# Kernel tuning notes

Measured on AMD Instinct MI355X. Metric: run time of the kernel, lower is better.

The kernel has to match this reference:

```python
import jax, jax.numpy as jnp
import numpy as np

B, C, T, L, H = 4, 512, 8, 512, 8


def _normalize(a, eps=1e-12):
    # F.normalize: x / max(||x||_2, eps) along last dim
    n = jnp.linalg.norm(a, axis=-1, keepdims=True)
    return a / jnp.maximum(n, eps)


def setup_inputs() -> dict:
    key = jax.random.key(0)
    ks = jax.random.split(key, 8)
    w = lambda k, shp: (jax.random.normal(k, shp, dtype=jnp.float32) * 0.02)
    return {
        "e": jax.random.normal(ks[0], (B, C, T, L), dtype=jnp.float32),
        "x": jax.random.normal(ks[1], (B, C, T, L), dtype=jnp.float32),
        "Wq": w(ks[2], (C, C)), "bq": jnp.zeros((C,), jnp.float32),
        "Wkv": w(ks[3], (2 * C, C)), "bkv": jnp.zeros((2 * C,), jnp.float32),
        "Wm": w(ks[4], (C, C)), "bm": jnp.zeros((C,), jnp.float32),
        "Wg1": w(ks[5], (C, C)), "bg1": jnp.zeros((C,), jnp.float32),
        "Wg2": w(ks[6], (H, C)), "bg2": jnp.zeros((H,), jnp.float32),
    }


def reference(e, x, Wq, bq, Wkv, bkv, Wm, bm, Wg1, bg1, Wg2, bg2):
    shortcut = x
    xp = jnp.transpose(x, (0, 2, 3, 1))  # (b,t,l,c)
    ep = jnp.transpose(e, (0, 2, 3, 1))  # (b,t,l,c)
    b, t, l, c = xp.shape
    hd = c // H

    # per-(b,t) head gating from pooled e (gate_weights1 == gate_weights in source)
    pooled = ep.mean(axis=2)  # (b,t,c)
    glog = jnp.tanh(pooled @ Wg1.T + bg1) @ Wg2.T + bg2  # (b,t,H)
    gw = jax.nn.softmax(glog, axis=-1)[..., None, None]  # (b,t,H,1,1)

    q = (ep @ Wq.T + bq).reshape(b, t, l, H, hd).transpose(0, 1, 3, 2, 4)  # (b,t,H,l,hd)
    q = _normalize(q)
    kv = (xp @ Wkv.T + bkv).reshape(b, t, l, 2 * H, hd).transpose(0, 1, 3, 2, 4)
    k, v = kv[:, :, :H], kv[:, :, H:]
    k = _normalize(k)
    v = _normalize(v) * gw  # pre-softmax value gating

    scale = jnp.float32(1.0 / np.sqrt(hd))
    att = jax.nn.softmax(jnp.einsum('bthid,bthjd->bthij', q, k) * scale, axis=-1)
    o = jnp.einsum('bthij,bthjd->bthid', att, v) * gw  # post-attention gating

    o = o.transpose(0, 1, 3, 2, 4).reshape(b, t, l, c)
    o = o @ Wm.T + bm
    return jnp.transpose(o, (0, 3, 1, 2)) + shortcut
```

## Files before the change

kernel.cpp:

```cpp
#include <hip/hip_runtime.h>
#include <hip/hip_bf16.h>
#include <math.h>

#define B_ 4
#define C_ 512
#define T_ 8
#define L_ 512
#define H_ 8
#define HD_ 64

typedef unsigned short ushort_t;
using short8 = __attribute__((ext_vector_type(8))) short;
using f4 = __attribute__((ext_vector_type(4))) float;

#define GLOAD_LDS(gp, lp)                                                      \
  __builtin_amdgcn_global_load_lds(                                            \
      (const __attribute__((address_space(1))) unsigned int*)(gp),             \
      (__attribute__((address_space(3))) unsigned int*)(lp), 16, 0, 0)

__device__ __forceinline__ unsigned pack_bf16(float a, float b) {
  union { float f; unsigned u; } ua, ub;
  ua.f = a; ub.f = b;
  unsigned ra = (ua.u + 0x7FFFu + ((ua.u >> 16) & 1u)) >> 16;
  unsigned rb = (ub.u + 0x7FFFu + ((ub.u >> 16) & 1u)) >> 16;
  return (rb << 16) | (ra & 0xFFFFu);
}
__device__ __forceinline__ unsigned pack2(float a, float b) {
  union { __hip_bfloat162 h; unsigned u; } cv;
  cv.h = __float22bfloat162_rn(make_float2(a, b));
  return cv.u;
}
__device__ __forceinline__ ushort_t bf16_1(float a) {
  union { float f; unsigned u; } ua; ua.f = a;
  return (ushort_t)((ua.u + 0x7FFFu + ((ua.u >> 16) & 1u)) >> 16);
}


__global__ __launch_bounds__(256) void gate1_kernel(const float* __restrict__ pooled,
                                                    const float* __restrict__ Wg1,
                                                    const float* __restrict__ bg1,
                                                    float* __restrict__ h1) {
  int w = threadIdx.x >> 6, lane = threadIdx.x & 63;
  int row = blockIdx.x * 4 + w;
  int bt = blockIdx.y;
  const float* wr = Wg1 + (size_t)row * C_;
  const float* pr = pooled + bt * C_;
  float s = 0.f;
#pragma unroll
  for (int i = 0; i < 8; ++i) s += wr[lane + i * 64] * pr[lane + i * 64];
#pragma unroll
  for (int off = 32; off > 0; off >>= 1) s += __shfl_down(s, off, 64);
  if (lane == 0) h1[bt * C_ + row] = tanhf(s + bg1[row]);
}

__global__ __launch_bounds__(256) void gate2_kernel(const float* __restrict__ h1,
                                                    const float* __restrict__ Wg2,
                                                    const float* __restrict__ bg2,
                                                    float* __restrict__ gwp) {
  __shared__ float part[256];
  __shared__ float gl[H_];
  int bt = blockIdx.x, tid = threadIdx.x;
  int h = tid >> 5, s = tid & 31;
  const float* w2 = Wg2 + (size_t)h * C_;
  const float* hb = h1 + bt * C_;
  float p = 0.f;
  for (int c = s; c < C_; c += 32) p += w2[c] * hb[c];
  part[tid] = p;
  __syncthreads();
  if (tid < H_) {
    float a = bg2[tid];
    for (int i = 0; i < 32; ++i) a += part[tid * 32 + i];
    gl[tid] = a;
  }
  __syncthreads();
  if (tid == 0) {
    float m = -1e30f;
    for (int i = 0; i < H_; ++i) m = fmaxf(m, gl[i]);
    float sum = 0.f;
    float ex[H_];
    for (int i = 0; i < H_; ++i) { ex[i] = expf(gl[i] - m); sum += ex[i]; }
    for (int i = 0; i < H_; ++i) gwp[bt * H_ + i] = ex[i] / sum;
  }
}

__global__ __launch_bounds__(256) void cvt3_kernel(const float* __restrict__ Wq,
                                                   const float* __restrict__ Wkv,
                                                   const float* __restrict__ Wm,
                                                   ushort_t* __restrict__ dWq,
                                                   ushort_t* __restrict__ dWkv,
                                                   ushort_t* __restrict__ dWm) {
  int i = (blockIdx.x * 256 + threadIdx.x) * 8;
  const float* s;
  ushort_t* d;
  int off;
  if (i < 262144)      { s = Wq;  d = dWq;  off = i; }
  else if (i < 786432) { s = Wkv; d = dWkv; off = i - 262144; }
  else                 { s = Wm;  d = dWm;  off = i - 786432; }
  float4 a = *(const float4*)(s + off);
  float4 b = *(const float4*)(s + off + 4);
  uint4 o;
  o.x = pack_bf16(a.x, a.y); o.y = pack_bf16(a.z, a.w);
  o.z = pack_bf16(b.x, b.y); o.w = pack_bf16(b.z, b.w);
  *(uint4*)(d + off) = o;
}

__global__ __launch_bounds__(256) void tconv_kernel(const float* __restrict__ e,
                                                    const float* __restrict__ x,
                                                    ushort_t* __restrict__ ebfT,
                                                    ushort_t* __restrict__ xbfT,
                                                    float* __restrict__ pooled) {
  __shared__ float tb[64][65];
  int tid = threadIdx.x;
  bool isE = blockIdx.z < 32;
  int bt = isE ? blockIdx.z : blockIdx.z - 32;
  const float* src = isE ? e : x;
  ushort_t* dst = isE ? ebfT : xbfT;
  int b = bt >> 3, t = bt & 7;
  int c0 = blockIdx.y * 64, l0 = blockIdx.x * 64;
  const float* sp = src + (((size_t)(b * C_ + c0) * T_) + t) * L_ + l0;
  int j = tid & 63, i0 = tid >> 6;
#pragma unroll
  for (int p = 0; p < 16; ++p) {
    int i = p * 4 + i0;
    tb[i][j] = sp[(size_t)i * (T_ * L_) + j];
  }
  __syncthreads();
  if (isE) {
    int c = tid >> 2, part = tid & 3;
    float s = 0.f;
#pragma unroll
    for (int k = 0; k < 16; ++k) s += tb[c][part * 16 + k];
    s += __shfl_down(s, 1);
    s += __shfl_down(s, 2);
    if (part == 0) atomicAdd(&pooled[bt * C_ + c0 + c], s * (1.0f / L_));
  }
  int ii = (tid & 31) * 2, jj0 = tid >> 5;
  ushort_t* dp = dst + ((size_t)bt * L_ + l0) * C_ + c0;
#pragma unroll
  for (int p = 0; p < 8; ++p) {
    int jj = p * 8 + jj0;
    *(unsigned*)(dp + (size_t)jj * C_ + ii) = pack_bf16(tb[ii][jj], tb[ii + 1][jj]);
  }
}

__global__ __launch_bounds__(256, 2) void gemm_mfma(
    const ushort_t* __restrict__ Aq, const ushort_t* __restrict__ BTq,
    const float* __restrict__ biasq, const ushort_t* __restrict__ Akv,
    const ushort_t* __restrict__ BTkv, const float* __restrict__ biaskv,
    int mode, float* __restrict__ Out, const float* __restrict__ resid,
    ushort_t* __restrict__ Qdst, ushort_t* __restrict__ Kdst,
    ushort_t* __restrict__ Vdst, const float* __restrict__ gwp) {
  __shared__ alignas(16) ushort_t As[2][128 * 32];
  __shared__ alignas(16) ushort_t Bs[2][128 * 32];
  int tid = threadIdx.x;
  int w = tid >> 6, lane = tid & 63, l15 = lane & 15, q = lane >> 4;
  int n0 = blockIdx.x * 128, bt = blockIdx.z;
  int wm = (w >> 1) * 64, wn = (w & 1) * 64;

  const ushort_t* A;
  const ushort_t* BT;
  const float* bias;
  int m0, lmode;
  if (mode == 3) {
    if (blockIdx.y < 4) {
      A = Aq; BT = BTq; bias = biasq; lmode = 1; m0 = blockIdx.y * 128;
    } else {
      A = Akv; BT = BTkv; bias = biaskv; lmode = 2; m0 = (blockIdx.y - 4) * 128;
    }
  } else {
    A = Aq; BT = BTq; bias = biasq; lmode = 0; m0 = blockIdx.y * 128;
  }
  const ushort_t* Bbt = BT + (size_t)bt * C_ * C_;

  int c0 = w * 64 + lane, c1 = 256 + w * 64 + lane;
  const ushort_t* ag0 = A + (size_t)(m0 + (c0 >> 2)) * 512 + (c0 & 3) * 8;
  const ushort_t* ag1 = A + (size_t)(m0 + (c1 >> 2)) * 512 + (c1 & 3) * 8;
  const ushort_t* bg0 = Bbt + (size_t)(n0 + (c0 >> 2)) * 512 + (c0 & 3) * 8;
  const ushort_t* bg1 = Bbt + (size_t)(n0 + (c1 >> 2)) * 512 + (c1 & 3) * 8;
  size_t lo0 = (size_t)(w * 64) * 8;
  size_t lo1 = (size_t)(256 + w * 64) * 8;

  f4 acc[4][4];
#pragma unroll
  for (int i = 0; i < 4; ++i)
#pragma unroll
    for (int j = 0; j < 4; ++j) acc[i][j] = (f4){0.f, 0.f, 0.f, 0.f};

  GLOAD_LDS(ag0, &As[0][lo0]);
  GLOAD_LDS(ag1, &As[0][lo1]);
  GLOAD_LDS(bg0, &Bs[0][lo0]);
  GLOAD_LDS(bg1, &Bs[0][lo1]);

  for (int it = 0; it < 16; ++it) {
    const int cur = it & 1;
    __syncthreads();
    if (it < 15) {
      const int k0 = (it + 1) * 32;
      GLOAD_LDS(ag0 + k0, &As[cur ^ 1][lo0]);
      GLOAD_LDS(ag1 + k0, &As[cur ^ 1][lo1]);
      GLOAD_LDS(bg0 + k0, &Bs[cur ^ 1][lo0]);
      GLOAD_LDS(bg1 + k0, &Bs[cur ^ 1][lo1]);
    }
    short8 af[4], bf[4];
#pragma unroll
    for (int mt = 0; mt < 4; ++mt)
      af[mt] = *(const short8*)&As[cur][(size_t)(wm + mt * 16 + l15) * 32 + q * 8];
#pragma unroll
    for (int nt = 0; nt < 4; ++nt)
      bf[nt] = *(const short8*)&Bs[cur][(size_t)(wn + nt * 16 + l15) * 32 + q * 8];
#pragma unroll
    for (int mt = 0; mt < 4; ++mt)
#pragma unroll
      for (int nt = 0; nt < 4; ++nt)
        acc[mt][nt] =
            __builtin_amdgcn_mfma_f32_16x16x32_bf16(af[mt], bf[nt], acc[mt][nt], 0, 0, 0);
  }

#pragma unroll
  for (int mt = 0; mt < 4; ++mt)
#pragma unroll
    for (int r = 0; r < 4; ++r) {
      float bb = bias[m0 + wm + mt * 16 + q * 4 + r];
#pragma unroll
      for (int nt = 0; nt < 4; ++nt) acc[mt][nt][r] += bb;
    }

  if (lmode == 0) {
    int b = bt >> 3, t = bt & 7;
    float* Ob = Out + (size_t)b * (C_ * T_ * L_) + (size_t)t * L_;
    const float* Rb = resid + (size_t)b * (C_ * T_ * L_) + (size_t)t * L_;
#pragma unroll
    for (int mt = 0; mt < 4; ++mt)
#pragma unroll
      for (int r = 0; r < 4; ++r) {
        size_t ro = (size_t)(m0 + wm + mt * 16 + q * 4 + r) * (T_ * L_);
#pragma unroll
        for (int nt = 0; nt < 4; ++nt) {
          int n = n0 + wn + nt * 16 + l15;
          Ob[ro + n] = acc[mt][nt][r] + Rb[ro + n];
        }
      }
    return;
  }

  float scale[4];
#pragma unroll
  for (int nt = 0; nt < 4; ++nt) {
    float s = 0.f;
#pragma unroll
    for (int mt = 0; mt < 4; ++mt)
#pragma unroll
      for (int r = 0; r < 4; ++r) s += acc[mt][nt][r] * acc[mt][nt][r];
    s += __shfl_xor(s, 16);
    s += __shfl_xor(s, 32);
    scale[nt] = s;
  }
  int hh = ((m0 + wm) >> 6) & 7;
  bool isv = (lmode == 2) && (m0 + wm >= 512);
  float mult = isv ? gwp[bt * H_ + hh]
                   : (lmode == 1 ? 0.125f * 1.44269504088896f : 1.0f);
#pragma unroll
  for (int nt = 0; nt < 4; ++nt)
    scale[nt] = mult / fmaxf(sqrtf(scale[nt]), 1e-12f);

  if (!isv) {
    ushort_t* Db = (lmode == 1 ? Qdst : Kdst) + (size_t)(bt * H_ + hh) * 512 * 64;
#pragma unroll
    for (int nt = 0; nt < 4; ++nt) {
      int l = n0 + wn + nt * 16 + l15;
      ushort_t* rowp = Db + (size_t)l * 64;
#pragma unroll
      for (int mt = 0; mt < 4; ++mt) {
        uint2 pk;
        pk.x = pack_bf16(acc[mt][nt][0] * scale[nt], acc[mt][nt][1] * scale[nt]);
        pk.y = pack_bf16(acc[mt][nt][2] * scale[nt], acc[mt][nt][3] * scale[nt]);
        *(uint2*)&rowp[mt * 16 + q * 4] = pk;
      }
    }
  } else {
    __syncthreads();
    ushort_t* scratch = &As[0][0] + (size_t)w * 1152;
    int d0 = (m0 - 512) + wm;
    ushort_t* Vb = Vdst + (size_t)(bt * H_ + hh) * 64 * 512;
#pragma unroll
    for (int mt = 0; mt < 4; ++mt) {
#pragma unroll
      for (int r = 0; r < 4; ++r) {
        int dr = q * 4 + r;
#pragma unroll
        for (int nt = 0; nt < 4; ++nt)
          scratch[dr * 72 + nt * 16 + l15] = bf16_1(acc[mt][nt][r] * scale[nt]);
      }
#pragma unroll
      for (int p = 0; p < 2; ++p) {
        int idx = p * 64 + lane;
        int row = idx >> 3, ch = idx & 7;
        uint4 v = *(const uint4*)&scratch[row * 72 + ch * 8];
        *(uint4*)(Vb + (size_t)(d0 + mt * 16 + row) * 512 + n0 + wn + ch * 8) = v;
      }
    }
  }
}

__global__ __launch_bounds__(256, 3) void attn_kernel(
    const ushort_t* __restrict__ Qbf, const ushort_t* __restrict__ Kbf,
    const ushort_t* __restrict__ Vbf, const float* __restrict__ gwp,
    ushort_t* __restrict__ obfT) {
  __shared__ alignas(16) ushort_t Ka[2][64 * 64];
  __shared__ alignas(16) ushort_t Va[2][64 * 64];

  int tid = threadIdx.x;
  int w = tid >> 6, lane = tid & 63, l15 = lane & 15, q = lane >> 4;
  int qb = blockIdx.x, h = blockIdx.y, bt = blockIdx.z;
  int iw = qb * 128 + w * 32;

  const ushort_t* Qg = Qbf + (size_t)(bt * H_ + h) * 512 * 64;
  const ushort_t* Kg = Kbf + (size_t)(bt * H_ + h) * 512 * 64;
  const ushort_t* Vg = Vbf + (size_t)(bt * H_ + h) * 64 * 512;

  int cA = tid, cB = tid + 256;
  const ushort_t* kgA = Kg + (size_t)(cA >> 3) * 64 + ((cA & 7) ^ ((cA >> 3) & 7)) * 8;
  const ushort_t* kgB = Kg + (size_t)(cB >> 3) * 64 + ((cB & 7) ^ ((cB >> 3) & 7)) * 8;
  const ushort_t* vgA = Vg + (size_t)(cA >> 3) * 512 + ((cA & 7) ^ ((cA >> 3) & 7)) * 8;
  const ushort_t* vgB = Vg + (size_t)(cB >> 3) * 512 + ((cB & 7) ^ ((cB >> 3) & 7)) * 8;

  short8 qf[2][2];
#pragma unroll
  for (int f = 0; f < 2; ++f) {
    const ushort_t* qrow = Qg + (size_t)(iw + f * 16 + l15) * 64;
    qf[f][0] = *(const short8*)&qrow[q * 8];
    qf[f][1] = *(const short8*)&qrow[32 + q * 8];
  }

  f4 acc[2][4];
#pragma unroll
  for (int f = 0; f < 2; ++f)
#pragma unroll
    for (int dt = 0; dt < 4; ++dt) acc[f][dt] = (f4){0.f, 0.f, 0.f, 0.f};
  float lsum[2] = {0.f, 0.f};
  bool hi_half = (lane >= 32);
  int qh2 = (q & 1) * 2;

  {
    GLOAD_LDS(kgA, Ka[0] + (size_t)(w * 64) * 8);
    GLOAD_LDS(kgB, Ka[0] + (size_t)(256 + w * 64) * 8);
    GLOAD_LDS(vgA, Va[0] + (size_t)(w * 64) * 8);
    GLOAD_LDS(vgB, Va[0] + (size_t)(256 + w * 64) * 8);
  }

  for (int jj = 0; jj < 8; ++jj) {
    const int cur = jj & 1;
    __syncthreads();
    if (jj < 7) {
      const int j0n = (jj + 1) * 64;
      GLOAD_LDS(kgA + (size_t)j0n * 64, Ka[cur ^ 1] + (size_t)(w * 64) * 8);
      GLOAD_LDS(kgB + (size_t)j0n * 64, Ka[cur ^ 1] + (size_t)(256 + w * 64) * 8);
      GLOAD_LDS(vgA + j0n, Va[cur ^ 1] + (size_t)(w * 64) * 8);
      GLOAD_LDS(vgB + j0n, Va[cur ^ 1] + (size_t)(256 + w * 64) * 8);
    }

    short8 kf[4][2], vf[2][4];
#pragma unroll
    for (int jt = 0; jt < 4; ++jt) {
      int row = jt * 16 + l15;
      int swz = row & 7;
      kf[jt][0] = *(const short8*)&Ka[cur][row * 64 + ((q ^ swz) * 8)];
      kf[jt][1] = *(const short8*)&Ka[cur][row * 64 + (((4 + q) ^ swz) * 8)];
    }
#pragma unroll
    for (int ks2 = 0; ks2 < 2; ++ks2)
#pragma unroll
      for (int dt = 0; dt < 4; ++dt) {
        int row = dt * 16 + l15;
        vf[ks2][dt] =
            *(const short8*)&Va[cur][row * 64 + (((ks2 * 4 + q) ^ (row & 7)) * 8)];
      }

#pragma unroll
    for (int f = 0; f < 2; ++f) {
      f4 sc[4];
#pragma unroll
      for (int jt = 0; jt < 4; ++jt) {
        f4 c = {0.f, 0.f, 0.f, 0.f};
        c = __builtin_amdgcn_mfma_f32_16x16x32_bf16(kf[jt][0], qf[f][0], c, 0, 0, 0);
        c = __builtin_amdgcn_mfma_f32_16x16x32_bf16(kf[jt][1], qf[f][1], c, 0, 0, 0);
        sc[jt] = c;
      }
      float ls = 0.f;
#pragma unroll
      for (int jt = 0; jt < 4; ++jt)
#pragma unroll
        for (int r = 0; r < 4; ++r) {
          float p = __builtin_exp2f(sc[jt][r]);
          sc[jt][r] = p;
          ls += p;
        }
      lsum[f] += ls;

      unsigned pk01[4], pk23[4];
#pragma unroll
      for (int jt = 0; jt < 4; ++jt) {
        pk01[jt] = pack2(sc[jt][0], sc[jt][1]);
        pk23[jt] = pack2(sc[jt][2], sc[jt][3]);
      }
#pragma unroll
      for (int ks2 = 0; ks2 < 2; ++ks2) {
        union { unsigned u[4]; short8 s; } bu;
#pragma unroll
        for (int r = 0; r < 4; ++r) {
          int src = (qh2 + (r >> 1)) * 16 + l15;
          unsigned pl = (r & 1) ? pk23[ks2 * 2] : pk01[ks2 * 2];
          unsigned ph = (r & 1) ? pk23[ks2 * 2 + 1] : pk01[ks2 * 2 + 1];
          unsigned lo = __shfl(pl, src);
          unsigned hi = __shfl(ph, src);
          bu.u[r] = hi_half ? hi : lo;
        }
#pragma unroll
        for (int dt = 0; dt < 4; ++dt)
          acc[f][dt] = __builtin_amdgcn_mfma_f32_16x16x32_bf16(vf[ks2][dt], bu.s,
                                                               acc[f][dt], 0, 0, 0);
      }
    }
  }

  float g = gwp[bt * H_ + h];
#pragma unroll
  for (int f = 0; f < 2; ++f) {
    float ls = lsum[f];
    ls += __shfl_xor(ls, 16);
    ls += __shfl_xor(ls, 32);
    float inv = g / ls;
    int iglob = iw + f * 16 + l15;
    ushort_t* ob = obfT + ((size_t)(bt * 512 + iglob)) * 512 + h * 64;
#pragma unroll
    for (int dt = 0; dt < 4; ++dt) {
      uint2 pk;
      pk.x = pack2(acc[f][dt][0] * inv, acc[f][dt][1] * inv);
      pk.y = pack2(acc[f][dt][2] * inv, acc[f][dt][3] * inv);
      *(uint2*)&ob[dt * 16 + q * 4] = pk;
    }
  }
}

extern "C" void kernel_launch(void* const* d_in, const int* in_sizes, int n_in,
                              void* d_out, int out_size, void* d_ws, size_t ws_size,
                              hipStream_t stream) {
  const float* e   = (const float*)d_in[0];
  const float* x   = (const float*)d_in[1];
  const float* Wq  = (const float*)d_in[2];
  const float* bq  = (const float*)d_in[3];
  const float* Wkv = (const float*)d_in[4];
  const float* bkv = (const float*)d_in[5];
  const float* Wm  = (const float*)d_in[6];
  const float* bm  = (const float*)d_in[7];
  const float* Wg1 = (const float*)d_in[8];
  const float* bg1 = (const float*)d_in[9];
  const float* Wg2 = (const float*)d_in[10];
  const float* bg2 = (const float*)d_in[11];
  float* out = (float*)d_out;

  float* ws = (float*)d_ws;
  float* pooled = ws;
  float* gwp    = ws + 16384;
  float* h1buf  = ws + 16640;
  float* fb     = ws + 33024;
  ushort_t* ebfT = (ushort_t*)(fb);
  ushort_t* xbfT = (ushort_t*)(fb + 1 * 4194304);
  ushort_t* Qbf  = (ushort_t*)(fb + 2 * 4194304);
  ushort_t* Kbf  = (ushort_t*)(fb + 3 * 4194304);
  ushort_t* Vbf  = (ushort_t*)(fb + 4 * 4194304);
  ushort_t* obfT = (ushort_t*)(fb + 5 * 4194304);
  ushort_t* Wqb  = (ushort_t*)(fb + 6 * 4194304);
  ushort_t* Wkvb = Wqb + 262144;
  ushort_t* Wmb  = Wkvb + 524288;

  hipMemsetAsync(pooled, 0, 16384 * sizeof(float), stream);
  cvt3_kernel<<<dim3(512), dim3(256), 0, stream>>>(Wq, Wkv, Wm, Wqb, Wkvb, Wmb);
  tconv_kernel<<<dim3(8, 8, 64), dim3(256), 0, stream>>>(e, x, ebfT, xbfT, pooled);
  gate1_kernel<<<dim3(128, 32), dim3(256), 0, stream>>>(pooled, Wg1, bg1, h1buf);
  gate2_kernel<<<dim3(32), dim3(256), 0, stream>>>(h1buf, Wg2, bg2, gwp);
  gemm_mfma<<<dim3(4, 12, 32), dim3(256), 0, stream>>>(
      Wqb, ebfT, bq, Wkvb, xbfT, bkv, 3, nullptr, nullptr, Qbf, Kbf, Vbf, gwp);
  attn_kernel<<<dim3(4, H_, 32), dim3(256), 0, stream>>>(Qbf, Kbf, Vbf, gwp, obfT);
  gemm_mfma<<<dim3(4, 4, 32), dim3(256), 0, stream>>>(
      Wmb, obfT, bm, nullptr, nullptr, nullptr, 0, out, x, nullptr, nullptr,
      nullptr, gwp);
}
```

Baseline: 259.5 us.

## Fuse prep kernels, drop memset/atomics, and fold gate softmax into attention

Merges the weight bf16 conversion into the transpose/pooling kernel. Per-block pooled partials replace atomics, so the memset is no longer needed, and gate1 reduces the partials. The second gating layer and softmax move into the attention kernel prologue, and the V-side gating is applied as the squared gate at the attention output. This cuts launches and global synchronisation points. In exchange, every attention block redundantly computes the gate dot products, and gate1 re-reduces the partials in each block.

```diff
diff --git a/kernel.cpp b/kernel.cpp
--- a/kernel.cpp
+++ b/kernel.cpp
@@ -36,81 +36,32 @@
 }
 
 
-__global__ __launch_bounds__(256) void gate1_kernel(const float* __restrict__ pooled,
-                                                    const float* __restrict__ Wg1,
-                                                    const float* __restrict__ bg1,
-                                                    float* __restrict__ h1) {
-  int w = threadIdx.x >> 6, lane = threadIdx.x & 63;
-  int row = blockIdx.x * 4 + w;
-  int bt = blockIdx.y;
-  const float* wr = Wg1 + (size_t)row * C_;
-  const float* pr = pooled + bt * C_;
-  float s = 0.f;
-#pragma unroll
-  for (int i = 0; i < 8; ++i) s += wr[lane + i * 64] * pr[lane + i * 64];
-#pragma unroll
-  for (int off = 32; off > 0; off >>= 1) s += __shfl_down(s, off, 64);
-  if (lane == 0) h1[bt * C_ + row] = tanhf(s + bg1[row]);
-}
-
-__global__ __launch_bounds__(256) void gate2_kernel(const float* __restrict__ h1,
-                                                    const float* __restrict__ Wg2,
-                                                    const float* __restrict__ bg2,
-                                                    float* __restrict__ gwp) {
-  __shared__ float part[256];
-  __shared__ float gl[H_];
-  int bt = blockIdx.x, tid = threadIdx.x;
-  int h = tid >> 5, s = tid & 31;
-  const float* w2 = Wg2 + (size_t)h * C_;
-  const float* hb = h1 + bt * C_;
-  float p = 0.f;
-  for (int c = s; c < C_; c += 32) p += w2[c] * hb[c];
-  part[tid] = p;
-  __syncthreads();
-  if (tid < H_) {
-    float a = bg2[tid];
-    for (int i = 0; i < 32; ++i) a += part[tid * 32 + i];
-    gl[tid] = a;
-  }
-  __syncthreads();
-  if (tid == 0) {
-    float m = -1e30f;
-    for (int i = 0; i < H_; ++i) m = fmaxf(m, gl[i]);
-    float sum = 0.f;
-    float ex[H_];
-    for (int i = 0; i < H_; ++i) { ex[i] = expf(gl[i] - m); sum += ex[i]; }
-    for (int i = 0; i < H_; ++i) gwp[bt * H_ + i] = ex[i] / sum;
-  }
-}
-
-__global__ __launch_bounds__(256) void cvt3_kernel(const float* __restrict__ Wq,
-                                                   const float* __restrict__ Wkv,
-                                                   const float* __restrict__ Wm,
-                                                   ushort_t* __restrict__ dWq,
-                                                   ushort_t* __restrict__ dWkv,
-                                                   ushort_t* __restrict__ dWm) {
-  int i = (blockIdx.x * 256 + threadIdx.x) * 8;
-  const float* s;
-  ushort_t* d;
-  int off;
-  if (i < 262144)      { s = Wq;  d = dWq;  off = i; }
-  else if (i < 786432) { s = Wkv; d = dWkv; off = i - 262144; }
-  else                 { s = Wm;  d = dWm;  off = i - 786432; }
-  float4 a = *(const float4*)(s + off);
-  float4 b = *(const float4*)(s + off + 4);
-  uint4 o;
-  o.x = pack_bf16(a.x, a.y); o.y = pack_bf16(a.z, a.w);
-  o.z = pack_bf16(b.x, b.y); o.w = pack_bf16(b.z, b.w);
-  *(uint4*)(d + off) = o;
-}
-
-__global__ __launch_bounds__(256) void tconv_kernel(const float* __restrict__ e,
-                                                    const float* __restrict__ x,
-                                                    ushort_t* __restrict__ ebfT,
-                                                    ushort_t* __restrict__ xbfT,
-                                                    float* __restrict__ pooled) {
+__global__ __launch_bounds__(256) void prep_kernel(
+    const float* __restrict__ e, const float* __restrict__ x,
+    const float* __restrict__ Wq, const float* __restrict__ Wkv,
+    const float* __restrict__ Wm, ushort_t* __restrict__ ebfT,
+    ushort_t* __restrict__ xbfT, ushort_t* __restrict__ dWq,
+    ushort_t* __restrict__ dWkv, ushort_t* __restrict__ dWm,
+    float* __restrict__ part) {
   __shared__ float tb[64][65];
   int tid = threadIdx.x;
+  if (blockIdx.z >= 64) {
+    int blk = (blockIdx.z - 64) * 64 + blockIdx.y * 8 + blockIdx.x;
+    int i = blk * 2048 + tid * 8;
+    const float* s;
+    ushort_t* d;
+    int off;
+    if (i < 262144)      { s = Wq;  d = dWq;  off = i; }
+    else if (i < 786432) { s = Wkv; d = dWkv; off = i - 262144; }
+    else                 { s = Wm;  d = dWm;  off = i - 786432; }
+    float4 a = *(const float4*)(s + off);
+    float4 b = *(const float4*)(s + off + 4);
+    uint4 o;
+    o.x = pack_bf16(a.x, a.y); o.y = pack_bf16(a.z, a.w);
+    o.z = pack_bf16(b.x, b.y); o.w = pack_bf16(b.z, b.w);
+    *(uint4*)(d + off) = o;
+    return;
+  }
   bool isE = blockIdx.z < 32;
   int bt = isE ? blockIdx.z : blockIdx.z - 32;
   const float* src = isE ? e : x;
@@ -126,13 +77,14 @@
   }
   __syncthreads();
   if (isE) {
-    int c = tid >> 2, part = tid & 3;
+    int c = tid >> 2, pt = tid & 3;
     float s = 0.f;
 #pragma unroll
-    for (int k = 0; k < 16; ++k) s += tb[c][part * 16 + k];
+    for (int k = 0; k < 16; ++k) s += tb[c][pt * 16 + k];
     s += __shfl_down(s, 1);
     s += __shfl_down(s, 2);
-    if (part == 0) atomicAdd(&pooled[bt * C_ + c0 + c], s * (1.0f / L_));
+    if (pt == 0)
+      part[((size_t)bt * 8 + blockIdx.x) * C_ + c0 + c] = s * (1.0f / L_);
   }
   int ii = (tid & 31) * 2, jj0 = tid >> 5;
   ushort_t* dp = dst + ((size_t)bt * L_ + l0) * C_ + c0;
@@ -141,6 +93,34 @@
     int jj = p * 8 + jj0;
     *(unsigned*)(dp + (size_t)jj * C_ + ii) = pack_bf16(tb[ii][jj], tb[ii + 1][jj]);
   }
+}
+
+__global__ __launch_bounds__(256) void gate1_kernel(const float* __restrict__ part,
+                                                    const float* __restrict__ Wg1,
+                                                    const float* __restrict__ bg1,
+                                                    float* __restrict__ h1) {
+  __shared__ float ps[C_];
+  int tid = threadIdx.x;
+  int w = tid >> 6, lane = tid & 63;
+  int bt = blockIdx.y;
+#pragma unroll
+  for (int half = 0; half < 2; ++half) {
+    int c = half * 256 + tid;
+    float s = 0.f;
+    const float* pb = part + (size_t)bt * 8 * C_ + c;
+#pragma unroll
+    for (int lb = 0; lb < 8; ++lb) s += pb[lb * C_];
+    ps[c] = s;
+  }
+  __syncthreads();
+  int row = blockIdx.x * 4 + w;
+  const float* wr = Wg1 + (size_t)row * C_;
+  float s = 0.f;
+#pragma unroll
+  for (int i = 0; i < 8; ++i) s += wr[lane + i * 64] * ps[lane + i * 64];
+#pragma unroll
+  for (int off = 32; off > 0; off >>= 1) s += __shfl_down(s, off, 64);
+  if (lane == 0) h1[bt * C_ + row] = tanhf(s + bg1[row]);
 }
 
 __global__ __launch_bounds__(256, 2) void gemm_mfma(
@@ -149,7 +129,7 @@
     const ushort_t* __restrict__ BTkv, const float* __restrict__ biaskv,
     int mode, float* __restrict__ Out, const float* __restrict__ resid,
     ushort_t* __restrict__ Qdst, ushort_t* __restrict__ Kdst,
-    ushort_t* __restrict__ Vdst, const float* __restrict__ gwp) {
+    ushort_t* __restrict__ Vdst) {
   __shared__ alignas(16) ushort_t As[2][128 * 32];
   __shared__ alignas(16) ushort_t Bs[2][128 * 32];
   int tid = threadIdx.x;
@@ -257,8 +237,7 @@
   }
   int hh = ((m0 + wm) >> 6) & 7;
   bool isv = (lmode == 2) && (m0 + wm >= 512);
-  float mult = isv ? gwp[bt * H_ + hh]
-                   : (lmode == 1 ? 0.125f * 1.44269504088896f : 1.0f);
+  float mult = (lmode == 1) ? 0.125f * 1.44269504088896f : 1.0f;
 #pragma unroll
   for (int nt = 0; nt < 4; ++nt)
     scale[nt] = mult / fmaxf(sqrtf(scale[nt]), 1e-12f);
@@ -304,10 +283,12 @@
 
 __global__ __launch_bounds__(256, 3) void attn_kernel(
     const ushort_t* __restrict__ Qbf, const ushort_t* __restrict__ Kbf,
-    const ushort_t* __restrict__ Vbf, const float* __restrict__ gwp,
+    const ushort_t* __restrict__ Vbf, const float* __restrict__ h1,
+    const float* __restrict__ Wg2, const float* __restrict__ bg2,
     ushort_t* __restrict__ obfT) {
   __shared__ alignas(16) ushort_t Ka[2][64 * 64];
   __shared__ alignas(16) ushort_t Va[2][64 * 64];
+  __shared__ float gsh;
 
   int tid = threadIdx.x;
   int w = tid >> 6, lane = tid & 63, l15 = lane & 15, q = lane >> 4;
@@ -317,6 +298,36 @@
   const ushort_t* Qg = Qbf + (size_t)(bt * H_ + h) * 512 * 64;
   const ushort_t* Kg = Kbf + (size_t)(bt * H_ + h) * 512 * 64;
   const ushort_t* Vg = Vbf + (size_t)(bt * H_ + h) * 64 * 512;
+
+  if (w == 0) {
+    const float* hb = h1 + bt * C_;
+    float lg[H_];
+#pragma unroll
+    for (int hh = 0; hh < H_; ++hh) {
+      const float* w2 = Wg2 + (size_t)hh * C_;
+      float p = 0.f;
+#pragma unroll
+      for (int i = 0; i < 8; ++i) p += w2[lane + i * 64] * hb[lane + i * 64];
+#pragma unroll
+      for (int off = 32; off > 0; off >>= 1) p += __shfl_down(p, off, 64);
+      lg[hh] = p;
+    }
+    if (lane == 0) {
+      float m = -1e30f;
+#pragma unroll
+      for (int i = 0; i < H_; ++i) {
+        lg[i] += bg2[i];
+        m = fmaxf(m, lg[i]);
+      }
+      float sum = 0.f;
+#pragma unroll
+      for (int i = 0; i < H_; ++i) {
+        lg[i] = expf(lg[i] - m);
+        sum += lg[i];
+      }
+      gsh = lg[h] / sum;
+    }
+  }
 
   int cA = tid, cB = tid + 256;
   const ushort_t* kgA = Kg + (size_t)(cA >> 3) * 64 + ((cA & 7) ^ ((cA >> 3) & 7)) * 8;
@@ -423,13 +434,14 @@
     }
   }
 
-  float g = gwp[bt * H_ + h];
+  float g = gsh;
+  float g2 = g * g;
 #pragma unroll
   for (int f = 0; f < 2; ++f) {
     float ls = lsum[f];
     ls += __shfl_xor(ls, 16);
     ls += __shfl_xor(ls, 32);
-    float inv = g / ls;
+    float inv = g2 / ls;
     int iglob = iw + f * 16 + l15;
     ushort_t* ob = obfT + ((size_t)(bt * 512 + iglob)) * 512 + h * 64;
 #pragma unroll
@@ -460,10 +472,9 @@
   float* out = (float*)d_out;
 
   float* ws = (float*)d_ws;
-  float* pooled = ws;
-  float* gwp    = ws + 16384;
-  float* h1buf  = ws + 16640;
-  float* fb     = ws + 33024;
+  float* part  = ws;
+  float* h1buf = ws + 131072;
+  float* fb    = ws + 147456;
   ushort_t* ebfT = (ushort_t*)(fb);
   ushort_t* xbfT = (ushort_t*)(fb + 1 * 4194304);
   ushort_t* Qbf  = (ushort_t*)(fb + 2 * 4194304);
@@ -474,15 +485,14 @@
   ushort_t* Wkvb = Wqb + 262144;
   ushort_t* Wmb  = Wkvb + 524288;
 
-  hipMemsetAsync(pooled, 0, 16384 * sizeof(float), stream);
-  cvt3_kernel<<<dim3(512), dim3(256), 0, stream>>>(Wq, Wkv, Wm, Wqb, Wkvb, Wmb);
-  tconv_kernel<<<dim3(8, 8, 64), dim3(256), 0, stream>>>(e, x, ebfT, xbfT, pooled);
-  gate1_kernel<<<dim3(128, 32), dim3(256), 0, stream>>>(pooled, Wg1, bg1, h1buf);
-  gate2_kernel<<<dim3(32), dim3(256), 0, stream>>>(h1buf, Wg2, bg2, gwp);
+  prep_kernel<<<dim3(8, 8, 72), dim3(256), 0, stream>>>(
+      e, x, Wq, Wkv, Wm, ebfT, xbfT, Wqb, Wkvb, Wmb, part);
+  gate1_kernel<<<dim3(128, 32), dim3(256), 0, stream>>>(part, Wg1, bg1, h1buf);
   gemm_mfma<<<dim3(4, 12, 32), dim3(256), 0, stream>>>(
-      Wqb, ebfT, bq, Wkvb, xbfT, bkv, 3, nullptr, nullptr, Qbf, Kbf, Vbf, gwp);
-  attn_kernel<<<dim3(4, H_, 32), dim3(256), 0, stream>>>(Qbf, Kbf, Vbf, gwp, obfT);
+      Wqb, ebfT, bq, Wkvb, xbfT, bkv, 3, nullptr, nullptr, Qbf, Kbf, Vbf);
+  attn_kernel<<<dim3(4, H_, 32), dim3(256), 0, stream>>>(Qbf, Kbf, Vbf, h1buf,
+                                                         Wg2, bg2, obfT);
   gemm_mfma<<<dim3(4, 4, 32), dim3(256), 0, stream>>>(
       Wmb, obfT, bm, nullptr, nullptr, nullptr, 0, out, x, nullptr, nullptr,
-      nullptr, gwp);
-}
+      nullptr);
+}
```

Result: no change. 257.2 us (-0.9%).
